# Performance work log

Hardware: AMD Instinct MI355X
Metric: run time of the kernel (lower is better)

## Reference

```python
import jax, jax.numpy as jnp
import numpy as np

NUM_HEADS = 16
TOP_K = 64


def setup_inputs() -> dict:
    key = jax.random.key(0)
    ks = jax.random.split(key, 9)
    B, S, E = 2, 1024, 1024
    x = jax.random.normal(ks[0], (B, S, E), jnp.float32)
    init = lambda k: jax.random.normal(k, (E, E), jnp.float32) * 0.02
    return {
        "x": x,
        "Wq": init(ks[1]), "bq": jnp.zeros((E,), jnp.float32),
        "Wk": init(ks[2]), "bk": jnp.zeros((E,), jnp.float32),
        "Wv": init(ks[3]), "bv": jnp.zeros((E,), jnp.float32),
        "Wo": init(ks[4]), "bo": jnp.zeros((E,), jnp.float32),
    }


def reference(x, Wq, bq, Wk, bk, Wv, bv, Wo, bo):
    B, S, E = x.shape
    H = NUM_HEADS
    hd = E // H
    scale = jnp.sqrt(jnp.float32(hd))

    def proj(W, b):  # torch nn.Linear: y = x @ W^T + b -> [B,H,S,hd]
        return (x @ W.T + b).reshape(B, S, H, hd).transpose(0, 2, 1, 3)

    q = proj(Wq, bq)
    k = proj(Wk, bk)
    v = proj(Wv, bv)

    # full scores, then per-query top-k selection (same math as the torch per-i loop)
    scores = jnp.einsum('bhqd,bhkd->bhqk', q, k) / scale          # [B,H,S,S]
    top_scores, top_idx = jax.lax.top_k(scores, TOP_K)            # [B,H,S,K]

    # gather top-k values: vg[b,h,q,j,:] = v[b,h, top_idx[b,h,q,j], :]
    vg = jnp.take_along_axis(v[:, :, None, :, :], top_idx[..., None], axis=3)  # [B,H,S,K,hd]

    # torch recomputes q . gathered_k / scale, which equals top_scores exactly
    w = jax.nn.softmax(top_scores, axis=-1)                       # [B,H,S,K]
    out = jnp.einsum('bhqk,bhqkd->bhqd', w, vg)                   # [B,H,S,hd]

    out = out.transpose(0, 2, 1, 3).reshape(B, S, E)
    return out @ Wo.T + bo
```

## Files before the change

### kernel.cpp

```cpp
#include <hip/hip_runtime.h>
#include <hip/hip_bf16.h>
#include <stdint.h>


typedef __bf16 bf16_t;
typedef bf16_t bf16x8 __attribute__((ext_vector_type(8)));
typedef bf16_t bf16x4 __attribute__((ext_vector_type(4)));
typedef float  f32x4  __attribute__((ext_vector_type(4)));

#define NB 2
#define SS 1024
#define EE 1024
#define NH 16
#define HD 64
#define NBH (NB*NH)
#define NX_ ((size_t)NB*SS*EE)
#define NW_ ((size_t)EE*EE)

__device__ __forceinline__ f32x4 mfma16(bf16x8 a, bf16x8 b, f32x4 c) {
  return __builtin_amdgcn_mfma_f32_16x16x32_bf16(a, b, c, 0, 0, 0);
}

__device__ __forceinline__ void split3(float x, bf16_t& h, bf16_t& m, bf16_t& l) {
  h = (bf16_t)x;
  float r = x - (float)h;
  m = (bf16_t)r;
  float r2 = r - (float)m;
  l = (bf16_t)r2;
}

__device__ __forceinline__ void wave_fence() {
  __builtin_amdgcn_wave_barrier();
  __builtin_amdgcn_s_waitcnt(0);
  __builtin_amdgcn_wave_barrier();
}

__device__ __forceinline__ void gld16(const bf16_t* g, bf16_t* l) {
  __builtin_amdgcn_global_load_lds(
      (const __attribute__((address_space(1))) void*)g,
      (__attribute__((address_space(3))) void*)l, 16, 0, 0);
}

__global__ __launch_bounds__(256) void presplit_all(
    const float* __restrict__ x,  const float* __restrict__ wq,
    const float* __restrict__ wk, const float* __restrict__ wv,
    const float* __restrict__ wo, bf16_t* __restrict__ base)
{
  const int blk = blockIdx.x;
  const float* src; bf16_t* h; size_t n; int i;
  if (blk < 2048)      { src = x;  h = base;                   n = NX_; i = blk;        }
  else if (blk < 3072) { src = wq; h = base + 3*NX_;           n = NW_; i = blk - 2048; }
  else if (blk < 4096) { src = wk; h = base + 3*NX_ + 3*NW_;   n = NW_; i = blk - 3072; }
  else if (blk < 5120) { src = wv; h = base + 3*NX_ + 6*NW_;   n = NW_; i = blk - 4096; }
  else                 { src = wo; h = base + 3*NX_ + 9*NW_;   n = NW_; i = blk - 5120; }
  bf16_t* m = h + n;
  bf16_t* l = m + n;
  int idx = i * 256 + threadIdx.x;
  float4 v = ((const float4*)src)[idx];
  float t[4] = { v.x, v.y, v.z, v.w };
  bf16x4 hv, mv, lv;
#pragma unroll
  for (int j = 0; j < 4; j++) {
    bf16_t a, b, c;
    split3(t[j], a, b, c);
    hv[j] = a; mv[j] = b; lv[j] = c;
  }
  ((bf16x4*)h)[idx] = hv;
  ((bf16x4*)m)[idx] = mv;
  ((bf16x4*)l)[idx] = lv;
}

__global__ __launch_bounds__(256, 2) void gemm_qk(
    const bf16_t* __restrict__ Ah, const bf16_t* __restrict__ Am,
    const bf16_t* __restrict__ Al,
    const bf16_t* __restrict__ Bqh, const bf16_t* __restrict__ Bqm,
    const bf16_t* __restrict__ Bql,
    const bf16_t* __restrict__ Bkh, const bf16_t* __restrict__ Bkm,
    const bf16_t* __restrict__ Bkl,
    const float* __restrict__ biasq, const float* __restrict__ biask,
    bf16_t* __restrict__ qH, bf16_t* __restrict__ qM, bf16_t* __restrict__ qL,
    bf16_t* __restrict__ kH, bf16_t* __restrict__ kM, bf16_t* __restrict__ kL)
{
  __shared__ bf16_t As[3][128 * 32];
  __shared__ bf16_t Bs[3][64 * 32];

  const int z = blockIdx.z;
  const bf16_t* AP[3] = { Ah, Am, Al };
  const bf16_t* BP[3] = { z ? Bkh : Bqh, z ? Bkm : Bqm, z ? Bkl : Bql };
  const float* bias = z ? biask : biasq;
  bf16_t* dH = z ? kH : qH;
  bf16_t* dM = z ? kM : qM;
  bf16_t* dL = z ? kL : qL;

  const int tid  = threadIdx.x;
  const int wv   = tid >> 6, lane = tid & 63;
  const int quad = lane >> 4, l16 = lane & 15;
  const int m0 = blockIdx.y * 128, n0 = blockIdx.x * 64;
  const int wm = (wv & 1) * 64, wn = (wv >> 1) * 32;

  const int arow = wv * 32 + (lane >> 2);
  const int brow = wv * 16 + (lane >> 2);
  const int q8   = (lane & 3) * 8;
  const size_t aoff0 = (size_t)(m0 + arow) * 1024 + q8;
  const size_t boff  = (size_t)(n0 + brow) * 1024 + q8;

  f32x4 accH0[4][2] = {};
  f32x4 accH1[4][2] = {};
  f32x4 accC [4][2] = {};

  for (int k0 = 0; k0 < 1024; k0 += 32) {
    __syncthreads();
#pragma unroll
    for (int L = 0; L < 3; L++) {
      gld16(AP[L] + aoff0 + k0,              &As[L][(wv * 32) * 32]);
      gld16(AP[L] + aoff0 + 16 * 1024 + k0,  &As[L][(wv * 32 + 16) * 32]);
      gld16(BP[L] + boff + k0,               &Bs[L][(wv * 16) * 32]);
    }
    __syncthreads();

    bf16x8 bfr[2][3];
#pragma unroll
    for (int nt = 0; nt < 2; nt++)
#pragma unroll
      for (int L = 0; L < 3; L++)
        bfr[nt][L] = *(const bf16x8*)&Bs[L][(wn + nt * 16 + l16) * 32 + quad * 8];

    const bool hi = (k0 >= 512);
#pragma unroll
    for (int mt = 0; mt < 4; mt++) {
      bf16x8 af[3];
#pragma unroll
      for (int L = 0; L < 3; L++)
        af[L] = *(const bf16x8*)&As[L][(wm + mt * 16 + l16) * 32 + quad * 8];
#pragma unroll
      for (int nt = 0; nt < 2; nt++) {
        f32x4& H = hi ? accH1[mt][nt] : accH0[mt][nt];
        H = mfma16(af[0], bfr[nt][0], H);
        f32x4 c = accC[mt][nt];
        c = mfma16(af[0], bfr[nt][1], c);
        c = mfma16(af[1], bfr[nt][0], c);
        c = mfma16(af[0], bfr[nt][2], c);
        c = mfma16(af[2], bfr[nt][0], c);
        c = mfma16(af[1], bfr[nt][1], c);
        accC[mt][nt] = c;
      }
    }
  }

#pragma unroll
  for (int mt = 0; mt < 4; mt++)
#pragma unroll
  for (int nt = 0; nt < 2; nt++)
#pragma unroll
  for (int r  = 0; r  < 4;  r++) {
    int gm = m0 + wm + mt * 16 + quad * 4 + r;
    int gn = n0 + wn + nt * 16 + l16;
    float v = (accH0[mt][nt][r] + accH1[mt][nt][r]) + accC[mt][nt][r] + bias[gn];
    int b_ = gm >> 10, s_ = gm & 1023, h_ = gn >> 6, d_ = gn & 63;
    size_t di = (((size_t)b_ * NH + h_) * SS + s_) * HD + d_;
    bf16_t hh, mm, ll;
    split3(v, hh, mm, ll);
    dH[di] = hh; dM[di] = mm; dL[di] = ll;
  }
}

template<int MODE>
__global__ __launch_bounds__(256, 4) void gemm_nl2(
    const bf16_t* __restrict__ Ah, const bf16_t* __restrict__ Am,
    const bf16_t* __restrict__ Bh, const bf16_t* __restrict__ Bm,
    const float* __restrict__ bias, float* __restrict__ dF)
{
  __shared__ bf16_t As[2][64 * 32];
  __shared__ bf16_t Bs[2][64 * 32];

  const bf16_t* AP[2] = { Ah, Am };
  const bf16_t* BP[2] = { Bh, Bm };

  const int tid  = threadIdx.x;
  const int wv   = tid >> 6, lane = tid & 63;
  const int quad = lane >> 4, l16 = lane & 15;
  const int m0 = blockIdx.y * 64, n0 = blockIdx.x * 64;
  const int wm = (wv & 1) * 32, wn = (wv >> 1) * 32;

  const int srow = wv * 16 + (lane >> 2);
  const int q8   = (lane & 3) * 8;
  const size_t aoff = (size_t)(m0 + srow) * 1024 + q8;
  const size_t boff = (size_t)(n0 + srow) * 1024 + q8;

  f32x4 accH0[2][2] = {};
  f32x4 accH1[2][2] = {};
  f32x4 accC [2][2] = {};

  for (int k0 = 0; k0 < 1024; k0 += 32) {
    __syncthreads();
#pragma unroll
    for (int L = 0; L < 2; L++) {
      gld16(AP[L] + aoff + k0, &As[L][(wv * 16) * 32]);
      gld16(BP[L] + boff + k0, &Bs[L][(wv * 16) * 32]);
    }
    __syncthreads();

    bf16x8 bfr[2][2];
#pragma unroll
    for (int nt = 0; nt < 2; nt++)
#pragma unroll
      for (int L = 0; L < 2; L++)
        bfr[nt][L] = *(const bf16x8*)&Bs[L][(wn + nt * 16 + l16) * 32 + quad * 8];

    const bool hi = (k0 >= 512);
#pragma unroll
    for (int mt = 0; mt < 2; mt++) {
      bf16x8 af[2];
#pragma unroll
      for (int L = 0; L < 2; L++)
        af[L] = *(const bf16x8*)&As[L][(wm + mt * 16 + l16) * 32 + quad * 8];
#pragma unroll
      for (int nt = 0; nt < 2; nt++) {
        f32x4& H = hi ? accH1[mt][nt] : accH0[mt][nt];
        H = mfma16(af[0], bfr[nt][0], H);
        f32x4 c = accC[mt][nt];
        c = mfma16(af[0], bfr[nt][1], c);
        c = mfma16(af[1], bfr[nt][0], c);
        accC[mt][nt] = c;
      }
    }
  }

#pragma unroll
  for (int mt = 0; mt < 2; mt++)
#pragma unroll
  for (int nt = 0; nt < 2; nt++)
#pragma unroll
  for (int r  = 0; r  < 4;  r++) {
    int gm = m0 + wm + mt * 16 + quad * 4 + r;
    int gn = n0 + wn + nt * 16 + l16;
    float v = (accH0[mt][nt][r] + accH1[mt][nt][r]) + accC[mt][nt][r] + bias[gn];
    if (MODE == 2) {
      dF[(size_t)gm * 1024 + gn] = v;
    } else {
      int b_ = gm >> 10, s_ = gm & 1023, h_ = gn >> 6, d_ = gn & 63;
      dF[(((size_t)b_ * NH + h_) * SS + s_) * HD + d_] = v;
    }
  }
}

__global__ __launch_bounds__(512, 4) void attn_topk(
    const bf16_t* __restrict__ qhg, const bf16_t* __restrict__ qmg,
    const bf16_t* __restrict__ qlg,
    const bf16_t* __restrict__ khg, const bf16_t* __restrict__ kmg,
    const bf16_t* __restrict__ klg,
    const float*  __restrict__ vg,
    bf16_t* __restrict__ attnH, bf16_t* __restrict__ attnM)
{
  __shared__ float sc[16 * 1028];

  const int tid  = threadIdx.x;
  const int wv   = tid >> 6, lane = tid & 63;
  const int quad = lane >> 4, l16 = lane & 15;
  const int xcd = blockIdx.x & 7;
  const int g   = blockIdx.x >> 3;
  const int bh  = xcd + 8 * (g >> 6);
  const int qt  = g & 63;
  const int b_ = bh >> 4, h_ = bh & 15;
  const int q0 = qt * 16;

  const size_t qbase = ((size_t)bh * SS + q0 + l16) * HD + quad * 8;
  bf16x8 aH[2], aM[2], aL[2];
#pragma unroll
  for (int ks = 0; ks < 2; ks++) {
    aH[ks] = *(const bf16x8*)(qhg + qbase + ks * 32);
    aM[ks] = *(const bf16x8*)(qmg + qbase + ks * 32);
    aL[ks] = *(const bf16x8*)(qlg + qbase + ks * 32);
  }

  const size_t kwb = ((size_t)bh * SS + wv * 128 + l16) * HD + quad * 8;
#pragma unroll 4
  for (int t2 = 0; t2 < 8; t2++) {
    const size_t kb = kwb + (size_t)t2 * 16 * HD;
    bf16x8 bH0 = *(const bf16x8*)(khg + kb);
    bf16x8 bH1 = *(const bf16x8*)(khg + kb + 32);
    bf16x8 bM0 = *(const bf16x8*)(kmg + kb);
    bf16x8 bM1 = *(const bf16x8*)(kmg + kb + 32);
    bf16x8 bL0 = *(const bf16x8*)(klg + kb);
    bf16x8 bL1 = *(const bf16x8*)(klg + kb + 32);
    f32x4 accA = {}, accB = {}, accC = {};
    accA = mfma16(aH[0], bH0, accA);
    accB = mfma16(aH[1], bH1, accB);
    accC = mfma16(aH[0], bM0, accC);
    accC = mfma16(aH[1], bM1, accC);
    accC = mfma16(aM[0], bH0, accC);
    accC = mfma16(aM[1], bH1, accC);
    accC = mfma16(aH[0], bL0, accC);
    accC = mfma16(aH[1], bL1, accC);
    accC = mfma16(aL[0], bH0, accC);
    accC = mfma16(aL[1], bH1, accC);
    accC = mfma16(aM[0], bM0, accC);
    accC = mfma16(aM[1], bM1, accC);
    int key = wv * 128 + t2 * 16 + l16;
#pragma unroll
    for (int r = 0; r < 4; r++)
      sc[(quad * 4 + r) * 1028 + key] = ((accA[r] + accB[r]) + accC[r]) * 0.125f;
  }
  __syncthreads();

  float fv[2][16];
#pragma unroll
  for (int i = 0; i < 16; i++) {
    fv[0][i] = sc[(2 * wv)     * 1028 + i * 64 + lane];
    fv[1][i] = sc[(2 * wv + 1) * 1028 + i * 64 + lane];
  }
  wave_fence();

  uint32_t* bins  = (uint32_t*)(sc + (2 * wv) * 1028);
  float*    candV = (float*)bins;
  ushort*   candI = (ushort*)(bins + 64);
  float*    selWw = sc + (2 * wv + 1) * 1028;
  ushort*   selIw = (ushort*)(selWw + 128);

  const uint64_t lt = (1ull << lane) - 1ull;
  for (int qi = 0; qi < 2; qi++) {
    const float* fq = fv[qi];
    *(uint4*)(bins + lane * 8)     = uint4{0, 0, 0, 0};
    *(uint4*)(bins + lane * 8 + 4) = uint4{0, 0, 0, 0};
    wave_fence();
#pragma unroll
    for (int i = 0; i < 16; i++) {
      int b = (int)fmaxf(0.f, fminf(511.f, fmaf(fq[i], 32.f, 256.f)));
      atomicAdd(bins + b, 1u);
    }
    wave_fence();
    int base = 504 - 8 * lane;
    uint4 h0 = *(const uint4*)(bins + base);
    uint4 h1 = *(const uint4*)(bins + base + 4);
    uint32_t s_l = h0.x + h0.y + h0.z + h0.w + h1.x + h1.y + h1.z + h1.w;
    uint32_t x = s_l;
#pragma unroll
    for (int off = 1; off < 64; off <<= 1) {
      uint32_t y = __shfl_up(x, off);
      if (lane >= off) x += y;
    }
    uint32_t P = x - s_l;
    uint32_t harr[8] = { h1.w, h1.z, h1.y, h1.x, h0.w, h0.z, h0.y, h0.x };
    uint32_t cb = P, G = 0;
    int foundc = -1;
#pragma unroll
    for (int c = 0; c < 8; c++) {
      uint32_t hc = harr[c];
      if (foundc < 0 && (int)cb < 64 && (int)(cb + hc) >= 64) { foundc = c; G = cb; }
      cb += hc;
    }
    uint64_t fm = __ballot(foundc >= 0);
    int src   = __ffsll((unsigned long long)fm) - 1;
    int Bstar = __shfl((foundc >= 0) ? (511 - 8 * lane - foundc) : 0, src);
    int Gs    = __shfl((int)G, src);
    int needed = 64 - Gs;
    wave_fence();

    int pos = 0, cT = 0;
#pragma unroll
    for (int i = 0; i < 16; i++) {
      int b = (int)fmaxf(0.f, fminf(511.f, fmaf(fq[i], 32.f, 256.f)));
      bool hi = b > Bstar;
      bool cd = (b == Bstar);
      uint64_t hm = __ballot(hi);
      uint64_t em = __ballot(cd);
      int p  = pos + (int)__popcll(hm & lt);
      int cp = cT  + (int)__popcll(em & lt);
      if (hi) { selWw[qi * 64 + p] = fq[i]; selIw[qi * 64 + p] = (ushort)(i * 64 + lane); }
      if (cd && cp < 64) { candV[cp] = fq[i]; candI[cp] = (ushort)(i * 64 + lane); }
      pos += (int)__popcll(hm);
      cT  += (int)__popcll(em);
    }
    wave_fence();
    int C = cT < 64 ? cT : 64;
    float mv = candV[lane];
    int   mi = candI[lane];
    int rank = 0;
    for (int i = 0; i < C; i++) {
      float ov = candV[i]; int oi = candI[i];
      rank += (ov > mv || (ov == mv && oi < mi)) ? 1 : 0;
    }
    bool take = (lane < C) && (rank < needed);
    uint64_t tm = __ballot(take);
    int slot = Gs + (int)__popcll(tm & lt);
    if (take) { selWw[qi * 64 + slot] = mv; selIw[qi * 64 + slot] = (ushort)mi; }
    wave_fence();
    float sv = selWw[qi * 64 + lane];
    float mx = sv;
#pragma unroll
    for (int off = 32; off >= 1; off >>= 1) mx = fmaxf(mx, __shfl_xor(mx, off));
    float e = __expf(sv - mx);
    float sum = e;
#pragma unroll
    for (int off = 32; off >= 1; off >>= 1) sum += __shfl_xor(sum, off);
    selWw[qi * 64 + lane] = e / sum;
    wave_fence();
  }

  {
    int ql = lane >> 5, jh = (lane >> 4) & 1, dblk = (lane & 15) * 4;
    const float* vb = vg + (size_t)bh * SS * HD;
    f32x4 a4 = {};
#pragma unroll
    for (int bch = 0; bch < 2; bch++) {
      float wreg[16]; int ireg[16];
#pragma unroll
      for (int j = 0; j < 16; j++) {
        int jj = jh * 32 + bch * 16 + j;
        wreg[j] = selWw[ql * 64 + jj];
        ireg[j] = selIw[ql * 64 + jj];
      }
#pragma unroll
      for (int j = 0; j < 16; j++) {
        f32x4 v4 = *(const f32x4*)(vb + (size_t)ireg[j] * HD + dblk);
        a4 += wreg[j] * v4;
      }
    }
#pragma unroll
    for (int c = 0; c < 4; c++) a4[c] += __shfl_xor(a4[c], 16);
    if (jh == 0) {
      int qg = q0 + 2 * wv + ql;
      size_t dofs = ((size_t)b_ * SS + qg) * EE + h_ * HD + dblk;
      bf16x4 oh, om;
#pragma unroll
      for (int j = 0; j < 4; j++) {
        bf16_t hh = (bf16_t)a4[j];
        oh[j] = hh;
        om[j] = (bf16_t)(a4[j] - (float)hh);
      }
      *(bf16x4*)(attnH + dofs) = oh;
      *(bf16x4*)(attnM + dofs) = om;
    }
  }
}

extern "C" void kernel_launch(void* const* d_in, const int* in_sizes, int n_in,
                              void* d_out, int out_size, void* d_ws, size_t ws_size,
                              hipStream_t stream)
{
  const float* x  = (const float*)d_in[0];
  const float* Wq = (const float*)d_in[1];
  const float* bq = (const float*)d_in[2];
  const float* Wk = (const float*)d_in[3];
  const float* bk = (const float*)d_in[4];
  const float* Wv = (const float*)d_in[5];
  const float* bv = (const float*)d_in[6];
  const float* Wo = (const float*)d_in[7];
  const float* bo = (const float*)d_in[8];

  bf16_t* base = (bf16_t*)d_ws;
  bf16_t *xh = base,            *xm = xh + NX_,  *xl = xm + NX_;
  bf16_t *wqh = base + 3*NX_,           *wqm = wqh + NW_, *wql = wqm + NW_;
  bf16_t *wkh = base + 3*NX_ + 3*NW_,   *wkm = wkh + NW_, *wkl = wkm + NW_;
  bf16_t *wvh = base + 3*NX_ + 6*NW_,   *wvm = wvh + NW_;
  bf16_t *woh = base + 3*NX_ + 9*NW_,   *wom = woh + NW_;
  bf16_t *p2 = base + 3*NX_ + 12*NW_;
  bf16_t *qh = p2,          *qm = qh + NX_, *ql = qm + NX_;
  bf16_t *kh = ql + NX_,    *km = kh + NX_, *kl = km + NX_;
  float  *vws = (float*)(kl + NX_);
  bf16_t *ath = (bf16_t*)(vws + NX_), *atm = ath + NX_;

  dim3 blk(256);
  presplit_all<<<dim3(6144), blk, 0, stream>>>(x, Wq, Wk, Wv, Wo, base);

  gemm_qk<<<dim3(EE / 64, (NB * SS) / 128, 2), blk, 0, stream>>>(
      xh, xm, xl, wqh, wqm, wql, wkh, wkm, wkl, bq, bk,
      qh, qm, ql, kh, km, kl);

  gemm_nl2<1><<<dim3(EE / 64, (NB * SS) / 64), blk, 0, stream>>>(
      xh, xm, wvh, wvm, bv, vws);

  attn_topk<<<dim3(NBH * (SS / 16)), dim3(512), 0, stream>>>(
      qh, qm, ql, kh, km, kl, vws, ath, atm);

  gemm_nl2<2><<<dim3(EE / 64, (NB * SS) / 64), blk, 0, stream>>>(
      ath, atm, woh, wom, bo, (float*)d_out);
}
```

Baseline: 317.3 us.

## Process two 16-query tiles per attention block to reuse loaded K fragments

Each attention block now handles 32 queries instead of 16. K fragments loaded from global memory feed MFMAs for both query groups, and the second group's scores are held in registers. After the first group's top-k and softmax tail runs, those scores are written back to shared memory for a second tail pass. This halves K global traffic per query and the block count, at the cost of more registers (launch bounds lowered to 3 blocks per CU) and a serialized second tail with extra barriers.

```diff
diff --git a/kernel.cpp b/kernel.cpp
--- a/kernel.cpp
+++ b/kernel.cpp
@@ -244,65 +244,11 @@
   }
 }
 
-__global__ __launch_bounds__(512, 4) void attn_topk(
-    const bf16_t* __restrict__ qhg, const bf16_t* __restrict__ qmg,
-    const bf16_t* __restrict__ qlg,
-    const bf16_t* __restrict__ khg, const bf16_t* __restrict__ kmg,
-    const bf16_t* __restrict__ klg,
-    const float*  __restrict__ vg,
+__device__ __forceinline__ void tail16(
+    float* __restrict__ sc, int wv, int lane,
+    const float* __restrict__ vb, int bh, int qgbase, int b_, int h_,
     bf16_t* __restrict__ attnH, bf16_t* __restrict__ attnM)
 {
-  __shared__ float sc[16 * 1028];
-
-  const int tid  = threadIdx.x;
-  const int wv   = tid >> 6, lane = tid & 63;
-  const int quad = lane >> 4, l16 = lane & 15;
-  const int xcd = blockIdx.x & 7;
-  const int g   = blockIdx.x >> 3;
-  const int bh  = xcd + 8 * (g >> 6);
-  const int qt  = g & 63;
-  const int b_ = bh >> 4, h_ = bh & 15;
-  const int q0 = qt * 16;
-
-  const size_t qbase = ((size_t)bh * SS + q0 + l16) * HD + quad * 8;
-  bf16x8 aH[2], aM[2], aL[2];
-#pragma unroll
-  for (int ks = 0; ks < 2; ks++) {
-    aH[ks] = *(const bf16x8*)(qhg + qbase + ks * 32);
-    aM[ks] = *(const bf16x8*)(qmg + qbase + ks * 32);
-    aL[ks] = *(const bf16x8*)(qlg + qbase + ks * 32);
-  }
-
-  const size_t kwb = ((size_t)bh * SS + wv * 128 + l16) * HD + quad * 8;
-#pragma unroll 4
-  for (int t2 = 0; t2 < 8; t2++) {
-    const size_t kb = kwb + (size_t)t2 * 16 * HD;
-    bf16x8 bH0 = *(const bf16x8*)(khg + kb);
-    bf16x8 bH1 = *(const bf16x8*)(khg + kb + 32);
-    bf16x8 bM0 = *(const bf16x8*)(kmg + kb);
-    bf16x8 bM1 = *(const bf16x8*)(kmg + kb + 32);
-    bf16x8 bL0 = *(const bf16x8*)(klg + kb);
-    bf16x8 bL1 = *(const bf16x8*)(klg + kb + 32);
-    f32x4 accA = {}, accB = {}, accC = {};
-    accA = mfma16(aH[0], bH0, accA);
-    accB = mfma16(aH[1], bH1, accB);
-    accC = mfma16(aH[0], bM0, accC);
-    accC = mfma16(aH[1], bM1, accC);
-    accC = mfma16(aM[0], bH0, accC);
-    accC = mfma16(aM[1], bH1, accC);
-    accC = mfma16(aH[0], bL0, accC);
-    accC = mfma16(aH[1], bL1, accC);
-    accC = mfma16(aL[0], bH0, accC);
-    accC = mfma16(aL[1], bH1, accC);
-    accC = mfma16(aM[0], bM0, accC);
-    accC = mfma16(aM[1], bM1, accC);
-    int key = wv * 128 + t2 * 16 + l16;
-#pragma unroll
-    for (int r = 0; r < 4; r++)
-      sc[(quad * 4 + r) * 1028 + key] = ((accA[r] + accB[r]) + accC[r]) * 0.125f;
-  }
-  __syncthreads();
-
   float fv[2][16];
 #pragma unroll
   for (int i = 0; i < 16; i++) {
@@ -399,7 +345,6 @@
 
   {
     int ql = lane >> 5, jh = (lane >> 4) & 1, dblk = (lane & 15) * 4;
-    const float* vb = vg + (size_t)bh * SS * HD;
     f32x4 a4 = {};
 #pragma unroll
     for (int bch = 0; bch < 2; bch++) {
@@ -419,7 +364,7 @@
 #pragma unroll
     for (int c = 0; c < 4; c++) a4[c] += __shfl_xor(a4[c], 16);
     if (jh == 0) {
-      int qg = q0 + 2 * wv + ql;
+      int qg = qgbase + 2 * wv + ql;
       size_t dofs = ((size_t)b_ * SS + qg) * EE + h_ * HD + dblk;
       bf16x4 oh, om;
 #pragma unroll
@@ -432,6 +377,107 @@
       *(bf16x4*)(attnM + dofs) = om;
     }
   }
+}
+
+__global__ __launch_bounds__(512, 3) void attn_topk(
+    const bf16_t* __restrict__ qhg, const bf16_t* __restrict__ qmg,
+    const bf16_t* __restrict__ qlg,
+    const bf16_t* __restrict__ khg, const bf16_t* __restrict__ kmg,
+    const bf16_t* __restrict__ klg,
+    const float*  __restrict__ vg,
+    bf16_t* __restrict__ attnH, bf16_t* __restrict__ attnM)
+{
+  __shared__ float sc[16 * 1028];
+
+  const int tid  = threadIdx.x;
+  const int wv   = tid >> 6, lane = tid & 63;
+  const int quad = lane >> 4, l16 = lane & 15;
+  const int xcd = blockIdx.x & 7;
+  const int g   = blockIdx.x >> 3;
+  const int bh  = xcd + 8 * (g >> 5);
+  const int qt  = g & 31;
+  const int b_ = bh >> 4, h_ = bh & 15;
+  const int q0 = qt * 32;
+
+  const size_t qb0 = ((size_t)bh * SS + q0 + l16) * HD + quad * 8;
+  bf16x8 aH[2][2], aM[2][2], aL[2][2];
+#pragma unroll
+  for (int grp = 0; grp < 2; grp++)
+#pragma unroll
+  for (int ks = 0; ks < 2; ks++) {
+    size_t qb = qb0 + (size_t)grp * 16 * HD + ks * 32;
+    aH[grp][ks] = *(const bf16x8*)(qhg + qb);
+    aM[grp][ks] = *(const bf16x8*)(qmg + qb);
+    aL[grp][ks] = *(const bf16x8*)(qlg + qb);
+  }
+
+  f32x4 sf1[8];
+  const size_t kwb = ((size_t)bh * SS + wv * 128 + l16) * HD + quad * 8;
+#pragma unroll
+  for (int t2 = 0; t2 < 8; t2++) {
+    const size_t kb = kwb + (size_t)t2 * 16 * HD;
+    bf16x8 bH0 = *(const bf16x8*)(khg + kb);
+    bf16x8 bH1 = *(const bf16x8*)(khg + kb + 32);
+    bf16x8 bM0 = *(const bf16x8*)(kmg + kb);
+    bf16x8 bM1 = *(const bf16x8*)(kmg + kb + 32);
+    bf16x8 bL0 = *(const bf16x8*)(klg + kb);
+    bf16x8 bL1 = *(const bf16x8*)(klg + kb + 32);
+    {
+      f32x4 accA = {}, accB = {}, accC = {};
+      accA = mfma16(aH[0][0], bH0, accA);
+      accB = mfma16(aH[0][1], bH1, accB);
+      accC = mfma16(aH[0][0], bM0, accC);
+      accC = mfma16(aH[0][1], bM1, accC);
+      accC = mfma16(aM[0][0], bH0, accC);
+      accC = mfma16(aM[0][1], bH1, accC);
+      accC = mfma16(aH[0][0], bL0, accC);
+      accC = mfma16(aH[0][1], bL1, accC);
+      accC = mfma16(aL[0][0], bH0, accC);
+      accC = mfma16(aL[0][1], bH1, accC);
+      accC = mfma16(aM[0][0], bM0, accC);
+      accC = mfma16(aM[0][1], bM1, accC);
+      int key = wv * 128 + t2 * 16 + l16;
+#pragma unroll
+      for (int r = 0; r < 4; r++)
+        sc[(quad * 4 + r) * 1028 + key] = ((accA[r] + accB[r]) + accC[r]) * 0.125f;
+    }
+    {
+      f32x4 accA = {}, accB = {}, accC = {};
+      accA = mfma16(aH[1][0], bH0, accA);
+      accB = mfma16(aH[1][1], bH1, accB);
+      accC = mfma16(aH[1][0], bM0, accC);
+      accC = mfma16(aH[1][1], bM1, accC);
+      accC = mfma16(aM[1][0], bH0, accC);
+      accC = mfma16(aM[1][1], bH1, accC);
+      accC = mfma16(aH[1][0], bL0, accC);
+      accC = mfma16(aH[1][1], bL1, accC);
+      accC = mfma16(aL[1][0], bH0, accC);
+      accC = mfma16(aL[1][1], bH1, accC);
+      accC = mfma16(aM[1][0], bM0, accC);
+      accC = mfma16(aM[1][1], bM1, accC);
+      f32x4 out;
+#pragma unroll
+      for (int r = 0; r < 4; r++)
+        out[r] = ((accA[r] + accB[r]) + accC[r]) * 0.125f;
+      sf1[t2] = out;
+    }
+  }
+  __syncthreads();
+
+  const float* vb = vg + (size_t)bh * SS * HD;
+  tail16(sc, wv, lane, vb, bh, q0, b_, h_, attnH, attnM);
+  __syncthreads();
+
+#pragma unroll
+  for (int t2 = 0; t2 < 8; t2++) {
+    int key = wv * 128 + t2 * 16 + l16;
+#pragma unroll
+    for (int r = 0; r < 4; r++)
+      sc[(quad * 4 + r) * 1028 + key] = sf1[t2][r];
+  }
+  __syncthreads();
+
+  tail16(sc, wv, lane, vb, bh, q0 + 16, b_, h_, attnH, attnM);
 }
 
 extern "C" void kernel_launch(void* const* d_in, const int* in_sizes, int n_in,
@@ -470,7 +516,7 @@
   gemm_nl2<1><<<dim3(EE / 64, (NB * SS) / 64), blk, 0, stream>>>(
       xh, xm, wvh, wvm, bv, vws);
 
-  attn_topk<<<dim3(NBH * (SS / 16)), dim3(512), 0, stream>>>(
+  attn_topk<<<dim3(NBH * (SS / 32)), dim3(512), 0, stream>>>(
       qh, qm, ql, kh, km, kl, vws, ath, atm);
 
   gemm_nl2<2><<<dim3(EE / 64, (NB * SS) / 64), blk, 0, stream>>>(
```

Result: slower. 350.5 us (+10.5%).
